# Performance work log

Measured on AMD Instinct MI355X. Metric: run time of the kernel, lower is better.

## Reference

```python
import jax, jax.numpy as jnp
import numpy as np

S = 2048      # sequence length
D = 2048      # d_model
H = 16        # n_heads
E = 128       # d_head


def setup_inputs() -> dict:
    key = jax.random.key(0)
    kx, kw = jax.random.split(key)
    x = jax.random.normal(kx, (S, D), dtype=jnp.float32)
    # xavier_normal for fan_in=D, fan_out=3*E per head
    std = float(np.sqrt(2.0 / (D + 3 * E)))
    w_qkv = jax.random.normal(kw, (H, D, 3 * E), dtype=jnp.float32) * std
    return {"x": x, "w_qkv": w_qkv}


def reference(x, w_qkv):
    # qkv: [h, s, 3e]
    qkv = jnp.einsum('sd,hde->hse', x, w_qkv)
    q, k, v = jnp.split(qkv, 3, axis=-1)            # each [h, s, e]
    scores = jnp.einsum('hse,hte->hst', q, k) / jnp.sqrt(jnp.asarray(E, x.dtype))
    attn = jax.nn.softmax(scores, axis=-1)          # [h, s, t]
    out = jnp.einsum('hst,hte->hse', attn, v)       # [h, s, e]
    # concat heads: [s, h*e]
    return out.transpose(1, 0, 2).reshape(x.shape[0], -1)
```

## Files before the change

kernel.cpp:

```cpp
#include <hip/hip_runtime.h>

#define SEQ 2048
#define DMODEL 2048
#define NHEAD 16
#define EHEAD 128
#define NE3 384

using short8 = __attribute__((ext_vector_type(8))) short;
using f32x4  = __attribute__((ext_vector_type(4))) float;

__device__ __forceinline__ unsigned short f32_to_bf16(float f) {
    unsigned int u = __float_as_uint(f);
    unsigned int rounding = 0x7fffu + ((u >> 16) & 1u);
    u += rounding;
    return (unsigned short)(u >> 16);
}

__device__ __forceinline__ void async_load16(const void* g, void* l) {
    __builtin_amdgcn_global_load_lds(
        (const __attribute__((address_space(1))) unsigned int*)g,
        (__attribute__((address_space(3))) unsigned int*)l, 16, 0, 0);
}

__global__ void cast_x_kernel(const float* __restrict__ x, unsigned short* __restrict__ xb) {
    int i = (blockIdx.x * blockDim.x + threadIdx.x) * 4;
    float4 v = *(const float4*)(x + i);
    ushort4 o = make_ushort4(f32_to_bf16(v.x), f32_to_bf16(v.y), f32_to_bf16(v.z), f32_to_bf16(v.w));
    *(ushort4*)(xb + i) = o;
}

__global__ void transpose_w_kernel(const float* __restrict__ w, unsigned short* __restrict__ wT) {
    __shared__ float tile[64][65];
    int h  = blockIdx.z;
    int d0 = blockIdx.x * 64;
    int n0 = blockIdx.y * 64;
    int t = threadIdx.x;
    int rr = t >> 4;
    int cc = (t & 15) * 4;
#pragma unroll
    for (int i = 0; i < 4; i++) {
        float4 v = *(const float4*)&w[(size_t)(h * DMODEL + d0 + rr + i * 16) * NE3 + n0 + cc];
        tile[rr + i * 16][cc + 0] = v.x;
        tile[rr + i * 16][cc + 1] = v.y;
        tile[rr + i * 16][cc + 2] = v.z;
        tile[rr + i * 16][cc + 3] = v.w;
    }
    __syncthreads();
#pragma unroll
    for (int i = 0; i < 4; i++) {
        int n = rr + i * 16;
        ushort4 o;
        o.x = f32_to_bf16(tile[cc + 0][n]);
        o.y = f32_to_bf16(tile[cc + 1][n]);
        o.z = f32_to_bf16(tile[cc + 2][n]);
        o.w = f32_to_bf16(tile[cc + 3][n]);
        *(ushort4*)&wT[(size_t)(h * NE3 + n0 + n) * DMODEL + d0 + cc] = o;
    }
}

__global__ __launch_bounds__(256, 2) void qkv_gemm128(
        const unsigned short* __restrict__ A,
        const unsigned short* __restrict__ B,
        unsigned short* __restrict__ Q,
        unsigned short* __restrict__ Kb,
        unsigned short* __restrict__ Vt) {
    __shared__ __attribute__((aligned(16))) unsigned short sA[128 * 32];
    __shared__ __attribute__((aligned(16))) unsigned short sB[128 * 32];
    const int mb = blockIdx.x, nb = blockIdx.y;
    const int tid = threadIdx.x;
    const int wave = tid >> 6, lane = tid & 63;
    const int r = lane & 15, q = lane >> 4;
    const int wm = wave & 1, wn = wave >> 1;

    const unsigned short* gA0 = A + (size_t)(mb * 128 + (tid >> 2)) * DMODEL + (tid & 3) * 8;
    const unsigned short* gA1 = gA0 + (size_t)64 * DMODEL;
    const unsigned short* gB0 = B + (size_t)(nb * 128 + (tid >> 2)) * DMODEL + (tid & 3) * 8;
    const unsigned short* gB1 = gB0 + (size_t)64 * DMODEL;
    unsigned short* lA0 = sA + wave * 512;
    unsigned short* lA1 = sA + 2048 + wave * 512;
    unsigned short* lB0 = sB + wave * 512;
    unsigned short* lB1 = sB + 2048 + wave * 512;

    f32x4 acc[4][4] = {};
    for (int k0 = 0; k0 < DMODEL; k0 += 32) {
        __syncthreads();
        async_load16(gA0 + k0, lA0);
        async_load16(gA1 + k0, lA1);
        async_load16(gB0 + k0, lB0);
        async_load16(gB1 + k0, lB1);
        __syncthreads();
        short8 a[4], b[4];
#pragma unroll
        for (int i = 0; i < 4; i++) a[i] = *(const short8*)&sA[(wm * 64 + i * 16 + r) * 32 + q * 8];
#pragma unroll
        for (int j = 0; j < 4; j++) b[j] = *(const short8*)&sB[(wn * 64 + j * 16 + r) * 32 + q * 8];
#pragma unroll
        for (int i = 0; i < 4; i++)
#pragma unroll
            for (int j = 0; j < 4; j++)
                acc[i][j] = __builtin_amdgcn_mfma_f32_16x16x32_bf16(a[i], b[j], acc[i][j], 0, 0, 0);
    }

    const int h = nb / 3, sel = nb % 3;
#pragma unroll
    for (int i = 0; i < 4; i++) {
#pragma unroll
        for (int j = 0; j < 4; j++) {
            const int row0 = mb * 128 + wm * 64 + i * 16 + q * 4;
            const int col  = wn * 64 + j * 16 + r;
            if (sel == 2) {
                ushort4 v;
                v.x = f32_to_bf16(acc[i][j][0]);
                v.y = f32_to_bf16(acc[i][j][1]);
                v.z = f32_to_bf16(acc[i][j][2]);
                v.w = f32_to_bf16(acc[i][j][3]);
                *(ushort4*)&Vt[((size_t)h * EHEAD + col) * SEQ + row0] = v;
            } else {
                unsigned short* dst = (sel == 0) ? Q : Kb;
#pragma unroll
                for (int reg = 0; reg < 4; reg++)
                    dst[((size_t)h * SEQ + row0 + reg) * EHEAD + col] = f32_to_bf16(acc[i][j][reg]);
            }
        }
    }
}

__global__ __launch_bounds__(256, 2) void flash_attn(
        const unsigned short* __restrict__ Qg,
        const unsigned short* __restrict__ Kg,
        const unsigned short* __restrict__ Vtg,
        float* __restrict__ out) {
    extern __shared__ __attribute__((aligned(16))) unsigned short lds[];
    unsigned short* sQ  = lds;
    unsigned short* sK0 = lds + 8192;
    unsigned short* sV0 = lds + 24576;

    const int tid = threadIdx.x;
    const int wave = tid >> 6, lane = tid & 63;
    const int r = lane & 15, q = lane >> 4;
    const int b = blockIdx.x;
    const int h  = (b & 7) + (((b >> 3) >> 5) << 3);
    const int m0 = ((b >> 3) & 31) * 64;

    const unsigned short* Qh  = Qg  + ((size_t)h * SEQ + m0) * EHEAD;
    const unsigned short* Kh0 = Kg  + (size_t)h * SEQ * EHEAD;
    const unsigned short* Vh  = Vtg + (size_t)h * EHEAD * SEQ;

#pragma unroll
    for (int c = 0; c < 4; c++)
        async_load16(Qh + (size_t)(tid >> 2) * EHEAD + c * 32 + (tid & 3) * 8,
                     sQ + c * 2048 + wave * 512);
#pragma unroll
    for (int c = 0; c < 4; c++)
        async_load16(Kh0 + (size_t)(tid >> 2) * EHEAD + c * 32 + (tid & 3) * 8,
                     sK0 + c * 2048 + wave * 512);
#pragma unroll
    for (int c = 0; c < 4; c++)
        async_load16(Vh + (size_t)((c & 1) * 64 + (tid >> 2)) * SEQ + (c >> 1) * 32 + (tid & 3) * 8,
                     sV0 + (c >> 1) * 4096 + (c & 1) * 2048 + wave * 512);
    __syncthreads();
    short8 aq[4];
#pragma unroll
    for (int kc = 0; kc < 4; kc++)
        aq[kc] = *(const short8*)&sQ[kc * 2048 + (wave * 16 + r) * 32 + q * 8];
    unsigned short* sP = sQ + wave * 1280;

    const float c1 = 0.12752405856f;
    f32x4 acc_o[8] = {};
    float l_i[4] = {};

    for (int it = 0; it < SEQ / 64; it++) {
        unsigned short* sKc = sK0 + (it & 1) * 8192;
        unsigned short* sVc = sV0 + (it & 1) * 8192;
        __syncthreads();
        if (it + 1 < SEQ / 64) {
            unsigned short* sKn = sK0 + ((it + 1) & 1) * 8192;
            unsigned short* sVn = sV0 + ((it + 1) & 1) * 8192;
            const unsigned short* Kh = Kh0 + (size_t)((it + 1) * 64) * EHEAD;
            const size_t koff = (size_t)(it + 1) * 64;
#pragma unroll
            for (int c = 0; c < 4; c++)
                async_load16(Kh + (size_t)(tid >> 2) * EHEAD + c * 32 + (tid & 3) * 8,
                             sKn + c * 2048 + wave * 512);
#pragma unroll
            for (int c = 0; c < 4; c++)
                async_load16(Vh + (size_t)((c & 1) * 64 + (tid >> 2)) * SEQ + koff + (c >> 1) * 32 + (tid & 3) * 8,
                             sVn + (c >> 1) * 4096 + (c & 1) * 2048 + wave * 512);
        }

        f32x4 s[4] = {};
#pragma unroll
        for (int j = 0; j < 4; j++)
#pragma unroll
            for (int kc = 0; kc < 4; kc++) {
                short8 bk = *(const short8*)&sKc[kc * 2048 + (j * 16 + r) * 32 + q * 8];
                s[j] = __builtin_amdgcn_mfma_f32_16x16x32_bf16(aq[kc], bk, s[j], 0, 0, 0);
            }

#pragma unroll
        for (int j = 0; j < 4; j++)
#pragma unroll
            for (int reg = 0; reg < 4; reg++) {
                float p = exp2f(s[j][reg] * c1);
                s[j][reg] = p;
                l_i[reg] += p;
            }

#pragma unroll
        for (int j = 0; j < 4; j++)
#pragma unroll
            for (int reg = 0; reg < 4; reg++)
                sP[(j >> 1) * 576 + (q * 4 + reg) * 36 + (j & 1) * 16 + r] = f32_to_bf16(s[j][reg]);

        short8 ap[2];
#pragma unroll
        for (int tk = 0; tk < 2; tk++)
            ap[tk] = *(const short8*)&sP[tk * 576 + r * 36 + q * 8];

#pragma unroll
        for (int j = 0; j < 8; j++)
#pragma unroll
            for (int tk = 0; tk < 2; tk++) {
                short8 bv = *(const short8*)&sVc[tk * 4096 + (j * 16 + r) * 32 + q * 8];
                acc_o[j] = __builtin_amdgcn_mfma_f32_16x16x32_bf16(ap[tk], bv, acc_o[j], 0, 0, 0);
            }
    }

    float inv[4];
#pragma unroll
    for (int reg = 0; reg < 4; reg++) {
        float l = l_i[reg];
        l += __shfl_xor(l, 1);
        l += __shfl_xor(l, 2);
        l += __shfl_xor(l, 4);
        l += __shfl_xor(l, 8);
        inv[reg] = 1.0f / l;
    }
#pragma unroll
    for (int j = 0; j < 8; j++)
#pragma unroll
        for (int reg = 0; reg < 4; reg++)
            out[(size_t)(m0 + wave * 16 + q * 4 + reg) * DMODEL + h * EHEAD + j * 16 + r] =
                acc_o[j][reg] * inv[reg];
}

extern "C" void kernel_launch(void* const* d_in, const int* in_sizes, int n_in,
                              void* d_out, int out_size, void* d_ws, size_t ws_size,
                              hipStream_t stream) {
    const float* x = (const float*)d_in[0];
    const float* w = (const float*)d_in[1];
    float* out = (float*)d_out;

    char* ws = (char*)d_ws;
    unsigned short* xb = (unsigned short*)(ws);
    unsigned short* wT = (unsigned short*)(ws + 8388608);
    unsigned short* Q  = (unsigned short*)(ws + 33554432);
    unsigned short* Kb = (unsigned short*)(ws + 41943040);
    unsigned short* Vt = (unsigned short*)(ws + 50331648);

    static bool attr_set = false;
    if (!attr_set) {
        hipFuncSetAttribute((const void*)flash_attn,
                            hipFuncAttributeMaxDynamicSharedMemorySize, 81920);
        attr_set = true;
    }

    cast_x_kernel<<<SEQ * DMODEL / (256 * 4), 256, 0, stream>>>(x, xb);
    transpose_w_kernel<<<dim3(DMODEL / 64, NE3 / 64, NHEAD), 256, 0, stream>>>(w, wT);
    qkv_gemm128<<<dim3(SEQ / 128, (NHEAD * NE3) / 128), 256, 0, stream>>>(xb, wT, Q, Kb, Vt);
    flash_attn<<<512, 256, 81920, stream>>>(Q, Kb, Vt, out);
}
```

Measured before the change: 229.5 us.

## Rework flash attention with 32x32 MFMA, swizzled LDS, register-resident P

Replaces the 16x16x32 MFMA formulation with 32x32x16 MFMAs using a 2x2 wave split over query rows and key columns, and computes S transposed so the probability tile can be turned into the next MFMA operand with cross-lane shuffles instead of a round trip through LDS. K, V and Q tiles move to an XOR-swizzled 128-wide LDS layout to avoid bank conflicts. Because each wave now covers only half of the key block, the partial outputs and row sums are reduced across wave pairs through LDS at the end. This aims to cut LDS traffic and instruction count per tile, at the price of an extra final reduction and more complex indexing.

```diff
diff --git a/kernel.cpp b/kernel.cpp
--- a/kernel.cpp
+++ b/kernel.cpp
@@ -8,6 +8,8 @@
 
 using short8 = __attribute__((ext_vector_type(8))) short;
 using f32x4  = __attribute__((ext_vector_type(4))) float;
+using f32x16 = __attribute__((ext_vector_type(16))) float;
+using uint4v = __attribute__((ext_vector_type(4))) unsigned int;
 
 __device__ __forceinline__ unsigned short f32_to_bf16(float f) {
     unsigned int u = __float_as_uint(f);
@@ -137,7 +139,8 @@
 
     const int tid = threadIdx.x;
     const int wave = tid >> 6, lane = tid & 63;
-    const int r = lane & 15, q = lane >> 4;
+    const int l31 = lane & 31, q2 = lane >> 5;
+    const int wm = wave >> 1, wn = wave & 1;
     const int b = blockIdx.x;
     const int h  = (b & 7) + (((b >> 3) >> 5) << 3);
     const int m0 = ((b >> 3) & 31) * 64;
@@ -146,102 +149,151 @@
     const unsigned short* Kh0 = Kg  + (size_t)h * SEQ * EHEAD;
     const unsigned short* Vh  = Vtg + (size_t)h * EHEAD * SEQ;
 
-#pragma unroll
-    for (int c = 0; c < 4; c++)
-        async_load16(Qh + (size_t)(tid >> 2) * EHEAD + c * 32 + (tid & 3) * 8,
-                     sQ + c * 2048 + wave * 512);
-#pragma unroll
-    for (int c = 0; c < 4; c++)
-        async_load16(Kh0 + (size_t)(tid >> 2) * EHEAD + c * 32 + (tid & 3) * 8,
-                     sK0 + c * 2048 + wave * 512);
-#pragma unroll
-    for (int c = 0; c < 4; c++)
-        async_load16(Vh + (size_t)((c & 1) * 64 + (tid >> 2)) * SEQ + (c >> 1) * 32 + (tid & 3) * 8,
-                     sV0 + (c >> 1) * 4096 + (c & 1) * 2048 + wave * 512);
+    const int qkRow = lane >> 4;
+    const int qkPos = lane & 15;
+    const int vRow  = lane >> 3;
+    const int vPos  = lane & 7;
+
+#pragma unroll
+    for (int c = 0; c < 4; c++) {
+        int u = wave * 4 + c;
+        int row = u * 4 + qkRow;
+        int ch = qkPos ^ (row & 7);
+        async_load16(Qh + (size_t)row * EHEAD + ch * 8, sQ + u * 512);
+        async_load16(Kh0 + (size_t)row * EHEAD + ch * 8, sK0 + u * 512);
+        int rv = u * 8 + vRow;
+        int cv = vPos ^ (rv & 7);
+        async_load16(Vh + (size_t)rv * SEQ + cv * 8, sV0 + u * 512);
+    }
     __syncthreads();
-    short8 aq[4];
-#pragma unroll
-    for (int kc = 0; kc < 4; kc++)
-        aq[kc] = *(const short8*)&sQ[kc * 2048 + (wave * 16 + r) * 32 + q * 8];
-    unsigned short* sP = sQ + wave * 1280;
+
+    short8 bq[8];
+    {
+        const int row = wm * 32 + l31;
+#pragma unroll
+        for (int kc = 0; kc < 8; kc++) {
+            int p = (kc * 2 + q2) ^ (row & 7);
+            bq[kc] = *(const short8*)&sQ[row * 128 + p * 8];
+        }
+    }
 
     const float c1 = 0.12752405856f;
-    f32x4 acc_o[8] = {};
-    float l_i[4] = {};
+    f32x16 acc_o[4] = {};
+    float l_acc = 0.f;
+    const int rowA = wn * 32 + l31;
 
     for (int it = 0; it < SEQ / 64; it++) {
         unsigned short* sKc = sK0 + (it & 1) * 8192;
         unsigned short* sVc = sV0 + (it & 1) * 8192;
-        __syncthreads();
         if (it + 1 < SEQ / 64) {
             unsigned short* sKn = sK0 + ((it + 1) & 1) * 8192;
             unsigned short* sVn = sV0 + ((it + 1) & 1) * 8192;
-            const unsigned short* Kh = Kh0 + (size_t)((it + 1) * 64) * EHEAD;
-            const size_t koff = (size_t)(it + 1) * 64;
-#pragma unroll
-            for (int c = 0; c < 4; c++)
-                async_load16(Kh + (size_t)(tid >> 2) * EHEAD + c * 32 + (tid & 3) * 8,
-                             sKn + c * 2048 + wave * 512);
-#pragma unroll
-            for (int c = 0; c < 4; c++)
-                async_load16(Vh + (size_t)((c & 1) * 64 + (tid >> 2)) * SEQ + koff + (c >> 1) * 32 + (tid & 3) * 8,
-                             sVn + (c >> 1) * 4096 + (c & 1) * 2048 + wave * 512);
-        }
-
-        f32x4 s[4] = {};
-#pragma unroll
-        for (int j = 0; j < 4; j++)
-#pragma unroll
-            for (int kc = 0; kc < 4; kc++) {
-                short8 bk = *(const short8*)&sKc[kc * 2048 + (j * 16 + r) * 32 + q * 8];
-                s[j] = __builtin_amdgcn_mfma_f32_16x16x32_bf16(aq[kc], bk, s[j], 0, 0, 0);
-            }
-
-#pragma unroll
-        for (int j = 0; j < 4; j++)
-#pragma unroll
-            for (int reg = 0; reg < 4; reg++) {
-                float p = exp2f(s[j][reg] * c1);
-                s[j][reg] = p;
-                l_i[reg] += p;
-            }
-
-#pragma unroll
-        for (int j = 0; j < 4; j++)
-#pragma unroll
-            for (int reg = 0; reg < 4; reg++)
-                sP[(j >> 1) * 576 + (q * 4 + reg) * 36 + (j & 1) * 16 + r] = f32_to_bf16(s[j][reg]);
-
-        short8 ap[2];
-#pragma unroll
-        for (int tk = 0; tk < 2; tk++)
-            ap[tk] = *(const short8*)&sP[tk * 576 + r * 36 + q * 8];
-
-#pragma unroll
-        for (int j = 0; j < 8; j++)
-#pragma unroll
-            for (int tk = 0; tk < 2; tk++) {
-                short8 bv = *(const short8*)&sVc[tk * 4096 + (j * 16 + r) * 32 + q * 8];
-                acc_o[j] = __builtin_amdgcn_mfma_f32_16x16x32_bf16(ap[tk], bv, acc_o[j], 0, 0, 0);
-            }
-    }
-
-    float inv[4];
-#pragma unroll
-    for (int reg = 0; reg < 4; reg++) {
-        float l = l_i[reg];
-        l += __shfl_xor(l, 1);
-        l += __shfl_xor(l, 2);
-        l += __shfl_xor(l, 4);
-        l += __shfl_xor(l, 8);
-        inv[reg] = 1.0f / l;
-    }
-#pragma unroll
-    for (int j = 0; j < 8; j++)
-#pragma unroll
-        for (int reg = 0; reg < 4; reg++)
-            out[(size_t)(m0 + wave * 16 + q * 4 + reg) * DMODEL + h * EHEAD + j * 16 + r] =
-                acc_o[j][reg] * inv[reg];
+            const unsigned short* Kh = Kh0 + (size_t)(it + 1) * 64 * EHEAD;
+#pragma unroll
+            for (int c = 0; c < 4; c++) {
+                int u = wave * 4 + c;
+                int row = u * 4 + qkRow;
+                int ch = qkPos ^ (row & 7);
+                async_load16(Kh + (size_t)row * EHEAD + ch * 8, sKn + u * 512);
+                int rv = u * 8 + vRow;
+                int cv = vPos ^ (rv & 7);
+                async_load16(Vh + (size_t)rv * SEQ + (it + 1) * 64 + cv * 8, sVn + u * 512);
+            }
+        }
+
+        f32x16 st = {};
+#pragma unroll
+        for (int kc = 0; kc < 8; kc++) {
+            int p = (kc * 2 + q2) ^ (rowA & 7);
+            short8 ak = *(const short8*)&sKc[rowA * 128 + p * 8];
+            st = __builtin_amdgcn_mfma_f32_32x32x16_bf16(ak, bq[kc], st, 0, 0, 0);
+        }
+
+        unsigned int pk[8];
+#pragma unroll
+        for (int t = 0; t < 8; t++) {
+            float p0 = exp2f(st[2 * t] * c1);
+            float p1 = exp2f(st[2 * t + 1] * c1);
+            l_acc += p0 + p1;
+            pk[t] = ((unsigned int)f32_to_bf16(p1) << 16) | (unsigned int)f32_to_bf16(p0);
+        }
+
+        short8 fr[2];
+#pragma unroll
+        for (int kc2 = 0; kc2 < 2; kc2++) {
+            unsigned int a0 = pk[kc2 * 4 + 0], a1 = pk[kc2 * 4 + 1];
+            unsigned int a2 = pk[kc2 * 4 + 2], a3 = pk[kc2 * 4 + 3];
+            unsigned int s0 = (unsigned int)__shfl_xor((int)a0, 32);
+            unsigned int s1 = (unsigned int)__shfl_xor((int)a1, 32);
+            unsigned int s2 = (unsigned int)__shfl_xor((int)a2, 32);
+            unsigned int s3 = (unsigned int)__shfl_xor((int)a3, 32);
+            uint4v t;
+            t.x = q2 ? s2 : a0;
+            t.y = q2 ? s3 : a1;
+            t.z = q2 ? a2 : s0;
+            t.w = q2 ? a3 : s1;
+            fr[kc2] = __builtin_bit_cast(short8, t);
+        }
+
+#pragma unroll
+        for (int et = 0; et < 4; et++) {
+            const int rowV = et * 32 + l31;
+#pragma unroll
+            for (int kc2 = 0; kc2 < 2; kc2++) {
+                int cch = wn * 4 + kc2 * 2 + q2;
+                int p = cch ^ (rowV & 7);
+                short8 bv = *(const short8*)&sVc[rowV * 64 + p * 8];
+                acc_o[et] = __builtin_amdgcn_mfma_f32_32x32x16_bf16(fr[kc2], bv, acc_o[et], 0, 0, 0);
+            }
+        }
+        __syncthreads();
+    }
+
+    l_acc += __shfl_xor(l_acc, 32);
+
+    float* fl = (float*)lds;
+#pragma unroll
+    for (int et = 0; et < 4; et++) {
+        if ((et >> 1) != wn) {
+#pragma unroll
+            for (int rg = 0; rg < 4; rg++) {
+                f32x4 v;
+                v[0] = acc_o[et][rg * 4 + 0];
+                v[1] = acc_o[et][rg * 4 + 1];
+                v[2] = acc_o[et][rg * 4 + 2];
+                v[3] = acc_o[et][rg * 4 + 3];
+                *(f32x4*)&fl[(size_t)(((wm * 4 + et) * 4 + rg) * 256) + lane * 4] = v;
+            }
+        }
+    }
+    fl[8192 + (wm * 2 + wn) * 32 + l31] = l_acc;
+    __syncthreads();
+
+    float invq[4][4];
+#pragma unroll
+    for (int rg = 0; rg < 4; rg++)
+#pragma unroll
+        for (int i = 0; i < 4; i++) {
+            int qy = i + 4 * q2 + 8 * rg;
+            float lt = fl[8192 + (wm * 2 + 0) * 32 + qy] + fl[8192 + (wm * 2 + 1) * 32 + qy];
+            invq[rg][i] = 1.0f / lt;
+        }
+
+#pragma unroll
+    for (int et2 = 0; et2 < 2; et2++) {
+        const int et = wn * 2 + et2;
+#pragma unroll
+        for (int rg = 0; rg < 4; rg++) {
+            f32x4 v = *(const f32x4*)&fl[(size_t)(((wm * 4 + et) * 4 + rg) * 256) + lane * 4];
+#pragma unroll
+            for (int i = 0; i < 4; i++) {
+                int reg = rg * 4 + i;
+                int mrow = i + 4 * q2 + 8 * rg;
+                out[(size_t)(m0 + wm * 32 + mrow) * DMODEL + h * EHEAD + et * 32 + l31] =
+                    (acc_o[et][reg] + v[i]) * invq[rg][i];
+            }
+        }
+    }
 }
 
 extern "C" void kernel_launch(void* const* d_in, const int* in_sizes, int n_in,
```

Result: slower. 430.7 us (+87.7%).
